# Kernel optimization log

Hardware: AMD Instinct MI355X
Metric: run time of the kernel (lower is better)

Reference implementation:

```python
import jax, jax.numpy as jnp
import numpy as np

PI = 3.1415926
MAX_V = 8  # max vertices of a quad-quad convex intersection
ALPHA, GAMMA, IOU_THRES = 0.25, 2.0, 0.5


def xyxy2xywh_a(b):
    cx = (b[..., 0] + b[..., 2]) * 0.5
    cy = (b[..., 1] + b[..., 3]) * 0.5
    w = b[..., 2] - b[..., 0]
    h = b[..., 3] - b[..., 1]
    return jnp.stack([cx, cy, w, h, b[..., 4]], -1)


def rbox_2_quad(b):
    # [N,5] (x1,y1,x2,y2,theta_deg) -> [N,4,2] corner quads
    x = xyxy2xywh_a(b)
    cx, cy, w, h, t = x[:, 0], x[:, 1], x[:, 2], x[:, 3], x[:, 4]
    th = t * (PI / 180.0)
    c, s = jnp.cos(th), jnp.sin(th)
    dx = jnp.array([-0.5, 0.5, 0.5, -0.5], b.dtype)
    dy = jnp.array([-0.5, -0.5, 0.5, 0.5], b.dtype)
    px = cx[:, None] + dx * w[:, None] * c[:, None] - dy * h[:, None] * s[:, None]
    py = cy[:, None] + dx * w[:, None] * s[:, None] + dy * h[:, None] * c[:, None]
    return jnp.stack([px, py], -1)


def min_area_square(b):
    cx = (b[:, 0] + b[:, 2]) * 0.5
    cy = (b[:, 1] + b[:, 3]) * 0.5
    s = jnp.maximum(b[:, 2] - b[:, 0], b[:, 3] - b[:, 1]) * 0.5
    return jnp.stack([cx - s, cy - s, cx + s, cy + s], 1)


def bbox_overlaps(a, b):
    # axis-aligned IoU matrix [N,M]
    lt = jnp.maximum(a[:, None, :2], b[None, :, :2])
    rb = jnp.minimum(a[:, None, 2:], b[None, :, 2:])
    wh = jnp.clip(rb - lt, 0.0)
    inter = wh[..., 0] * wh[..., 1]
    area_a = (a[:, 2] - a[:, 0]) * (a[:, 3] - a[:, 1])
    area_b = (b[:, 2] - b[:, 0]) * (b[:, 3] - b[:, 1])
    return inter / (area_a[:, None] + area_b[None, :] - inter + 1e-6)


def points_in_quads(pts, quads):
    # pointsJf: pts [A,2] inside convex quads [G,4,2] -> [A,G] {0,1}
    e = jnp.roll(quads, -1, axis=1) - quads  # [G,4,2]
    rel = pts[:, None, None, :] - quads[None]  # [A,G,4,2]
    cr = e[None, ..., 0] * rel[..., 1] - e[None, ..., 1] * rel[..., 0]
    inside = jnp.all(cr >= 0, -1) | jnp.all(cr <= 0, -1)
    return inside.astype(pts.dtype)


def _signed_area2(q):
    return jnp.sum(q[:, 0] * jnp.roll(q[:, 1], -1) - jnp.roll(q[:, 0], -1) * q[:, 1])


def _quad_inter_area(q1, q2):
    # Sutherland-Hodgman clipping of quad q1 by convex quad q2, fixed 8-vertex buffer
    q1 = jnp.where(_signed_area2(q1) < 0, q1[::-1], q1)
    q2 = jnp.where(_signed_area2(q2) < 0, q2[::-1], q2)
    poly = jnp.zeros((MAX_V, 2), q1.dtype).at[:4].set(q1)
    edges = jnp.stack([q2, jnp.roll(q2, -1, axis=0)], 1)  # [4,2,2]

    def clip(carry, edge):
        poly, n = carry
        a, b = edge[0], edge[1]
        idx = jnp.arange(MAX_V)
        nidx = jnp.where(idx + 1 < n, idx + 1, 0)
        cur, nxt = poly, poly[nidx]
        d = b - a
        dc = d[0] * (cur[:, 1] - a[1]) - d[1] * (cur[:, 0] - a[0])
        dn = d[0] * (nxt[:, 1] - a[1]) - d[1] * (nxt[:, 0] - a[0])
        denom = dc - dn
        t = dc / jnp.where(jnp.abs(denom) < 1e-12, 1e-12, denom)
        inter = cur + t[:, None] * (nxt - cur)
        active = idx < n
        keep_cur = active & (dc >= 0)
        keep_int = active & ((dc >= 0) != (dn >= 0))
        pts = jnp.stack([cur, inter], 1).reshape(2 * MAX_V, 2)
        flags = jnp.stack([keep_cur, keep_int], 1).reshape(-1)
        pos = jnp.where(flags, jnp.cumsum(flags) - 1, MAX_V)
        newpoly = jnp.zeros((MAX_V + 1, 2), poly.dtype).at[pos].set(pts)[:MAX_V]
        return (newpoly, flags.sum()), None

    (poly, n), _ = jax.lax.scan(clip, (poly, jnp.int32(4)), edges)
    idx = jnp.arange(MAX_V)
    nidx = jnp.where(idx + 1 < n, idx + 1, 0)
    contrib = poly[:, 0] * poly[nidx, 1] - poly[nidx, 0] * poly[:, 1]
    area = 0.5 * jnp.abs(jnp.sum(jnp.where(idx < n, contrib, 0.0)))
    return jnp.where(n >= 3, area, 0.0)


def rbox_overlaps(quads_a, quads_g, gate, thresh=0.1):
    area_a = 0.5 * jnp.abs(jax.vmap(_signed_area2)(quads_a))
    area_g = 0.5 * jnp.abs(jax.vmap(_signed_area2)(quads_g))
    inter = jax.vmap(lambda qa: jax.vmap(lambda qg: _quad_inter_area(qa, qg))(quads_g))(quads_a)
    iou = inter / (area_a[:, None] + area_g[None, :] - inter + 1e-6)
    return jnp.where(gate > thresh, iou, 0.0)


def encode(anchors, gt):
    a = xyxy2xywh_a(anchors)
    g = xyxy2xywh_a(gt)
    dx = (g[:, 0] - a[:, 0]) / a[:, 2]
    dy = (g[:, 1] - a[:, 1]) / a[:, 3]
    dw = jnp.log(g[:, 2] / a[:, 2])
    dh = jnp.log(g[:, 3] / a[:, 3])
    dt = (g[:, 4] - a[:, 4]) * (PI / 180.0)
    return jnp.stack([dx, dy, dw, dh, dt], 1)


def decode(anchors, deltas):
    a = xyxy2xywh_a(anchors)
    cx = a[..., 0] + deltas[..., 0] * a[..., 2]
    cy = a[..., 1] + deltas[..., 1] * a[..., 3]
    w = a[..., 2] * jnp.exp(deltas[..., 2])
    h = a[..., 3] * jnp.exp(deltas[..., 3])
    t = a[..., 4] + deltas[..., 4] * (180.0 / PI)
    return jnp.stack([cx, cy, w, h, t], -1)


def smooth_l1(x, t, beta=1.0 / 9):
    diff = jnp.abs(x - t)
    return jnp.where(diff < beta, 0.5 * diff * diff / beta, diff - 0.5 * beta)


def _forward(classifications, regressions, anchors, annotations):
    B = classifications.shape[0]
    _ = decode(anchors, regressions)  # all_pred_boxes (unused when func='smooth')
    cls_losses, reg_losses = [], []
    for j in range(B):
        cls = jnp.clip(classifications[j], 1e-4, 1.0 - 1e-4)
        anch = anchors[j]
        gtb = annotations[j, :, :5]
        labels = annotations[j, :, 5].astype(jnp.int32)
        indicator = bbox_overlaps(min_area_square(anch), min_area_square(gtb))
        centers = xyxy2xywh_a(anch)[:, :2]
        quads_g = rbox_2_quad(gtb)
        inside = points_in_quads(centers, quads_g)
        quads_a = rbox_2_quad(anch)
        ious = rbox_overlaps(quads_a, quads_g, inside * indicator)  # [A,G]
        iou_max = ious.max(1)
        iou_argmax = ious.argmax(1)
        pos = iou_max >= IOU_THRES
        max_gt = ious.max(0)
        argmax_gt = ious.argmax(0)
        low = (max_gt < IOU_THRES).astype(jnp.int32)
        pos = (pos.astype(jnp.int32).at[argmax_gt].max(low)).astype(bool)
        num_pos = pos.sum()
        C = cls.shape[1]
        onehot = jax.nn.one_hot(labels[iou_argmax], C, dtype=cls.dtype)
        tgt = -jnp.ones_like(cls)
        tgt = jnp.where((iou_max < IOU_THRES - 0.1)[:, None], 0.0, tgt)
        tgt = jnp.where(pos[:, None], onehot, tgt)
        af = jnp.where(tgt == 1.0, ALPHA, 1.0 - ALPHA)
        fw = af * jnp.where(tgt == 1.0, 1.0 - cls, cls) ** GAMMA
        bce = -(tgt * jnp.log(cls + 1e-6) + (1.0 - tgt) * jnp.log(1.0 - cls + 1e-6))
        cls_loss = jnp.where(tgt != -1.0, fw * bce, 0.0).sum() / jnp.maximum(num_pos.astype(cls.dtype), 1.0)
        cls_losses.append(cls_loss)
        reg_t = encode(anch, gtb[iou_argmax])
        l = smooth_l1(regressions[j], reg_t)
        denom = (jnp.maximum(num_pos, 1) * l.shape[1]).astype(l.dtype)
        reg_loss = jnp.where(num_pos > 0, (l * pos[:, None].astype(l.dtype)).sum() / denom, 0.0)
        reg_losses.append(reg_loss)
    loss_cls = 5.0 * jnp.stack(cls_losses).mean(keepdims=True)
    loss_reg = 2.0 * jnp.stack(reg_losses).mean(keepdims=True)
    return loss_cls, loss_reg


def setup_inputs() -> dict:
    key = jax.random.key(0)
    ks = jax.random.split(key, 8)
    B, A, G, C = 2, 32768, 32, 15
    cls = jax.random.uniform(ks[0], (B, A, C), jnp.float32)
    reg = jax.random.normal(ks[1], (B, A, 5), jnp.float32) * 0.1
    ac = jax.random.uniform(ks[2], (B, A, 2), jnp.float32, 0.0, 1024.0)
    awh = jax.random.uniform(ks[3], (B, A, 2), jnp.float32, 16.0, 256.0)
    anchors = jnp.concatenate([ac - awh * 0.5, ac + awh * 0.5, jnp.zeros((B, A, 1), jnp.float32)], -1)
    gc = jax.random.uniform(ks[4], (B, G, 2), jnp.float32, 64.0, 960.0)
    gwh = jax.random.uniform(ks[5], (B, G, 2), jnp.float32, 24.0, 300.0)
    gt = jax.random.uniform(ks[6], (B, G, 1), jnp.float32, -90.0, 90.0)
    glab = jax.random.randint(ks[7], (B, G, 1), 0, C).astype(jnp.float32)
    annotations = jnp.concatenate([gc - gwh * 0.5, gc + gwh * 0.5, gt, glab], -1)
    return {"classifications": cls, "regressions": reg, "anchors": anchors, "annotations": annotations}


def reference(classifications, regressions, anchors, annotations):
    return _forward(classifications, regressions, anchors, annotations)
```

## Files before the change

kernel.cpp:

```cpp
#include <hip/hip_runtime.h>

#define A_N 32768
#define G_N 32
#define C_N 15
#define APB 256
#define H_N 4
#define BPB (A_N / APB)
#define DEG2RAD ((float)(3.1415926 / 180.0))
#define BETA (1.0f / 9.0f)

typedef unsigned long long ull;

template <int NIN>
__device__ __forceinline__ int clip_pass(float ax, float ay, float dx, float dy,
                                         float (&PX)[8], float (&PY)[8], int n) {
  constexpr int NOUT = (NIN + 1 < 8) ? NIN + 1 : 8;
  float d[NIN];
#pragma unroll
  for (int i = 0; i < NIN; ++i)
    d[i] = dx * (PY[i] - ay) - dy * (PX[i] - ax);
  float NX[NOUT], NY[NOUT];
#pragma unroll
  for (int i = 0; i < NOUT; ++i) { NX[i] = 0.f; NY[i] = 0.f; }
  int m = 0;
#pragma unroll
  for (int i = 0; i < NIN; ++i) {
    if (i < n) {
      bool w = (i + 1 < n);
      float dn = w ? d[(i + 1) % NIN] : d[0];
      float xn = w ? PX[(i + 1) % NIN] : PX[0];
      float yn = w ? PY[(i + 1) % NIN] : PY[0];
      bool kc = (d[i] >= 0.f);
      bool kn = (dn >= 0.f);
      if (kc) {
#pragma unroll
        for (int o = 0; o < NOUT; ++o)
          if (o <= 2 * i && m == o) { NX[o] = PX[i]; NY[o] = PY[i]; }
        ++m;
      }
      if (kc != kn) {
        float den = d[i] - dn;
        if (fabsf(den) < 1e-12f) den = 1e-12f;
        float t = d[i] / den;
        float ix = PX[i] + t * (xn - PX[i]);
        float iy = PY[i] + t * (yn - PY[i]);
#pragma unroll
        for (int o = 0; o < NOUT; ++o)
          if (o <= 2 * i + 1 && m == o) { NX[o] = ix; NY[o] = iy; }
        ++m;
      }
    }
  }
#pragma unroll
  for (int i = 0; i < NOUT; ++i) { PX[i] = NX[i]; PY[i] = NY[i]; }
#pragma unroll
  for (int i = NOUT; i < 8; ++i) { PX[i] = 0.f; PY[i] = 0.f; }
  return m;
}

__global__ __launch_bounds__(1024) void k_fused(
    const float* __restrict__ cls_in, const float* __restrict__ reg_in,
    const float* __restrict__ anchors, const float* __restrict__ annot,
    ull* __restrict__ gpart, ull* __restrict__ rowpack,
    float* __restrict__ cls_part, float* __restrict__ reg_part,
    int* __restrict__ cnt_part) {
  int j = blockIdx.x >> 7;
  int blk = blockIdx.x & (BPB - 1);
  int tid = threadIdx.x;
  int la = tid & (APB - 1);
  int h = tid >> 8;
  int a = blk * APB + la;
  size_t ia = (size_t)j * A_N + a;

  __shared__ float4 g_sqv[G_N];
  __shared__ float2 g_meta[G_N];
  __shared__ float4 g_vx[G_N], g_vy[G_N];
  __shared__ float4 a_qx[APB], a_qy[APB];
  __shared__ float a_area[APB];
  __shared__ ull rowbest[APB];
  __shared__ ull colmax[G_N];
  __shared__ unsigned short list[APB * G_N];
  __shared__ int cnt;
  __shared__ int lab[G_N];
  __shared__ float gcx[G_N], gcy[G_N], gw2[G_N], gh2[G_N], gth[G_N];
  __shared__ float w1[16], w2[16];
  __shared__ int w3[16];

  float pcv[4];
  {
    const float* c = cls_in + ia * C_N;
#pragma unroll
    for (int k = 0; k < 4; ++k) {
      int ci = h * 4 + k;
      pcv[k] = (ci < C_N) ? c[ci] : 0.f;
    }
  }
  float rvv[5];
  if (h == 0) {
    const float* r = reg_in + ia * 5;
#pragma unroll
    for (int i = 0; i < 5; ++i) rvv[i] = r[i];
  } else {
#pragma unroll
    for (int i = 0; i < 5; ++i) rvv[i] = 0.f;
  }

  if (tid == 0) cnt = 0;
  if (tid < APB) rowbest[tid] = 0xFFFFFFFFull;
  if (tid < G_N) colmax[tid] = 0xFFFFFFFFull;

  if (tid < G_N) {
    const float* g = annot + ((size_t)j * G_N + tid) * 6;
    float x1 = g[0], y1 = g[1], x2 = g[2], y2 = g[3], t = g[4];
    float cxx = (x1 + x2) * 0.5f, cyy = (y1 + y2) * 0.5f;
    float w = x2 - x1, hh = y2 - y1;
    gcx[tid] = cxx; gcy[tid] = cyy; gw2[tid] = w; gh2[tid] = hh; gth[tid] = t;
    lab[tid] = (int)g[5];
    float th = t * DEG2RAD;
    float c = cosf(th), s = sinf(th);
    const float ddx[4] = {-0.5f, 0.5f, 0.5f, -0.5f};
    const float ddy[4] = {-0.5f, -0.5f, 0.5f, 0.5f};
    float px[4], py[4];
#pragma unroll
    for (int k = 0; k < 4; ++k) {
      px[k] = cxx + ddx[k] * w * c - ddy[k] * hh * s;
      py[k] = cyy + ddx[k] * w * s + ddy[k] * hh * c;
    }
    float s2 = 0.f;
#pragma unroll
    for (int k = 0; k < 4; ++k)
      s2 += px[k] * py[(k + 1) & 3] - px[(k + 1) & 3] * py[k];
    if (s2 < 0.f) {
      g_vx[tid] = make_float4(px[3], px[2], px[1], px[0]);
      g_vy[tid] = make_float4(py[3], py[2], py[1], py[0]);
    } else {
      g_vx[tid] = make_float4(px[0], px[1], px[2], px[3]);
      g_vy[tid] = make_float4(py[0], py[1], py[2], py[3]);
    }
    float half = fmaxf(w, hh) * 0.5f;
    float sx1 = cxx - half, sy1 = cyy - half, sx2 = cxx + half, sy2 = cyy + half;
    g_sqv[tid] = make_float4(sx1, sy1, sx2, sy2);
    g_meta[tid] = make_float2((sx2 - sx1) * (sy2 - sy1), 0.5f * fabsf(s2));
  }

  const float* an = anchors + ia * 5;
  float ax1 = an[0], ay1 = an[1], ax2 = an[2], ay2 = an[3], at = an[4];
  float acx = (ax1 + ax2) * 0.5f, acy = (ay1 + ay2) * 0.5f;
  float aw = ax2 - ax1, ah = ay2 - ay1;
  float ath = at * DEG2RAD;
  float ac = cosf(ath), asn = sinf(ath);
  {
    const float ddx[4] = {-0.5f, 0.5f, 0.5f, -0.5f};
    const float ddy[4] = {-0.5f, -0.5f, 0.5f, 0.5f};
    float apx[4], apy[4];
#pragma unroll
    for (int k = 0; k < 4; ++k) {
      apx[k] = acx + ddx[k] * aw * ac - ddy[k] * ah * asn;
      apy[k] = acy + ddx[k] * aw * asn + ddy[k] * ah * ac;
    }
    float s2a = 0.f;
#pragma unroll
    for (int k = 0; k < 4; ++k)
      s2a += apx[k] * apy[(k + 1) & 3] - apx[(k + 1) & 3] * apy[k];
    if (s2a < 0.f) {
      float tx = apx[0], ty = apy[0];
      apx[0] = apx[3]; apy[0] = apy[3]; apx[3] = tx; apy[3] = ty;
      tx = apx[1]; ty = apy[1];
      apx[1] = apx[2]; apy[1] = apy[2]; apx[2] = tx; apy[2] = ty;
    }
    if (h == 0) {
      a_qx[la] = make_float4(apx[0], apx[1], apx[2], apx[3]);
      a_qy[la] = make_float4(apy[0], apy[1], apy[2], apy[3]);
      a_area[la] = 0.5f * fabsf(s2a);
    }
  }
  float half = fmaxf(aw, ah) * 0.5f;
  float asx1 = acx - half, asy1 = acy - half, asx2 = acx + half, asy2 = acy + half;
  float asarea = (asx2 - asx1) * (asy2 - asy1);
  __syncthreads();

#pragma unroll
  for (int gg = 0; gg < G_N / H_N; ++gg) {
    int g = h * (G_N / H_N) + gg;
    float4 sq = g_sqv[g];
    float2 meta = g_meta[g];
    float ltx = fmaxf(asx1, sq.x);
    float lty = fmaxf(asy1, sq.y);
    float rbx = fminf(asx2, sq.z);
    float rby = fminf(asy2, sq.w);
    float iw = fmaxf(rbx - ltx, 0.f);
    float ih = fmaxf(rby - lty, 0.f);
    float inter_s = iw * ih;
    float ind = inter_s / (asarea + meta.x - inter_s + 1e-6f);
    float4 vx = g_vx[g], vy = g_vy[g];
    float cr0 = (vx.y - vx.x) * (acy - vy.x) - (vy.y - vy.x) * (acx - vx.x);
    float cr1 = (vx.z - vx.y) * (acy - vy.y) - (vy.z - vy.y) * (acx - vx.y);
    float cr2 = (vx.w - vx.z) * (acy - vy.z) - (vy.w - vy.z) * (acx - vx.z);
    float cr3 = (vx.x - vx.w) * (acy - vy.w) - (vy.x - vy.w) * (acx - vx.w);
    bool pall = (cr0 >= 0.f) & (cr1 >= 0.f) & (cr2 >= 0.f) & (cr3 >= 0.f);
    bool nall = (cr0 <= 0.f) & (cr1 <= 0.f) & (cr2 <= 0.f) & (cr3 <= 0.f);
    if ((pall || nall) && ind > 0.1f) {
      int p = atomicAdd(&cnt, 1);
      list[p] = (unsigned short)((la << 5) | g);
    }
  }
  __syncthreads();

  int np = cnt;
  for (int i = tid; i < np; i += 1024) {
    int ent = list[i];
    int ca = ent >> 5, g = ent & 31;
    float4 aqx = a_qx[ca], aqy = a_qy[ca];
    float PX[8], PY[8];
    PX[0] = aqx.x; PX[1] = aqx.y; PX[2] = aqx.z; PX[3] = aqx.w;
    PY[0] = aqy.x; PY[1] = aqy.y; PY[2] = aqy.z; PY[3] = aqy.w;
#pragma unroll
    for (int k = 4; k < 8; ++k) { PX[k] = 0.f; PY[k] = 0.f; }
    float4 gvx = g_vx[g], gvy = g_vy[g];
    int n = 4;
    n = clip_pass<4>(gvx.x, gvy.x, gvx.y - gvx.x, gvy.y - gvy.x, PX, PY, n);
    n = clip_pass<5>(gvx.y, gvy.y, gvx.z - gvx.y, gvy.z - gvy.y, PX, PY, n);
    n = clip_pass<6>(gvx.z, gvy.z, gvx.w - gvx.z, gvy.w - gvy.z, PX, PY, n);
    n = clip_pass<7>(gvx.w, gvy.w, gvx.x - gvx.w, gvy.x - gvy.w, PX, PY, n);
    float s = 0.f;
#pragma unroll
    for (int k = 0; k < 8; ++k) {
      if (k < n) {
        float xn = (k + 1 < n) ? PX[(k + 1) & 7] : PX[0];
        float yn = (k + 1 < n) ? PY[(k + 1) & 7] : PY[0];
        s += PX[k] * yn - xn * PY[k];
      }
    }
    float inter = (n >= 3) ? 0.5f * fabsf(s) : 0.f;
    float v = inter / (a_area[ca] + g_meta[g].y - inter + 1e-6f);
    ull pr = ((ull)__float_as_uint(v) << 32) | (unsigned)(~(unsigned)g);
    atomicMax(&rowbest[ca], pr);
    unsigned ga = (unsigned)(blk * APB + ca);
    ull pc = ((ull)__float_as_uint(v) << 32) | (unsigned)(~ga);
    atomicMax(&colmax[g], pc);
  }
  __syncthreads();

  ull rb = rowbest[la];
  float im = __uint_as_float((unsigned)(rb >> 32));
  int arg = (int)(~(unsigned)rb);
  int p = (im >= 0.5f) ? 1 : 0;

  if (h == 0) rowpack[ia] = rb;
  if (tid < G_N)
    gpart[((size_t)j * BPB + blk) * G_N + tid] = colmax[tid];

  int lb = lab[arg];
  float csum = 0.f;
  bool bg = (im < 0.4f);
  if (p || bg) {
#pragma unroll
    for (int k = 0; k < 4; ++k) {
      int ci = h * 4 + k;
      if (ci < C_N) {
        float pc = fminf(fmaxf(pcv[k], 1e-4f), 0.9999f);
        bool tgt1 = p && (ci == lb);
        if (tgt1)
          csum += 0.25f * (1.f - pc) * (1.f - pc) * (-__logf(pc + 1e-6f));
        else
          csum += 0.75f * pc * pc * (-__logf(1.f - pc + 1e-6f));
      }
    }
  }

  float rsum = 0.f;
  if (p && h == 0) {
    float t5[5];
    t5[0] = (gcx[arg] - acx) / aw;
    t5[1] = (gcy[arg] - acy) / ah;
    t5[2] = __logf(gw2[arg] / aw);
    t5[3] = __logf(gh2[arg] / ah);
    t5[4] = (gth[arg] - at) * DEG2RAD;
#pragma unroll
    for (int i = 0; i < 5; ++i) {
      float d = fabsf(rvv[i] - t5[i]);
      rsum += (d < BETA) ? (0.5f * d * d / BETA) : (d - 0.5f * BETA);
    }
  }
  int pcnt = (h == 0) ? p : 0;

  float v1 = csum, v2 = rsum;
  int v3 = pcnt;
#pragma unroll
  for (int off = 32; off; off >>= 1) {
    v1 += __shfl_xor(v1, off);
    v2 += __shfl_xor(v2, off);
    v3 += __shfl_xor(v3, off);
  }
  int wv = tid >> 6, ln = tid & 63;
  if (ln == 0) { w1[wv] = v1; w2[wv] = v2; w3[wv] = v3; }
  __syncthreads();
  if (tid == 0) {
    float t1 = 0.f, t2 = 0.f;
    int t3 = 0;
#pragma unroll
    for (int k = 0; k < 16; ++k) { t1 += w1[k]; t2 += w2[k]; t3 += w3[k]; }
    cls_part[blockIdx.x] = t1;
    reg_part[blockIdx.x] = t2;
    cnt_part[blockIdx.x] = t3;
  }
}

__global__ __launch_bounds__(256) void k_fix(
    const float* __restrict__ cls_in, const float* __restrict__ reg_in,
    const float* __restrict__ anchors, const float* __restrict__ annot,
    const ull* __restrict__ gpart, const ull* __restrict__ rowpack,
    const float* __restrict__ cls_part, const float* __restrict__ reg_part,
    const int* __restrict__ cnt_part, float* __restrict__ out, int B) {
  int tid = threadIdx.x;
  __shared__ ull sred[8][G_N];
  __shared__ int fanchor[G_N], owner[G_N];
  __shared__ float dcs[G_N], drs[G_N];
  __shared__ int dct[G_N];
  __shared__ float bd_c[8], bd_r[8];
  __shared__ int bd_n[8];
  __shared__ float s1[256], s2[256];
  __shared__ int s3[256];

  for (int j = 0; j < B; ++j) {
    {
      int g = tid & 31, chunk = tid >> 5;
      const ull* gp = gpart + (size_t)j * BPB * G_N;
      ull m = 0;
#pragma unroll
      for (int b = 0; b < BPB / 8; ++b) {
        ull v = gp[(size_t)(chunk * (BPB / 8) + b) * G_N + g];
        m = v > m ? v : m;
      }
      sred[chunk][g] = m;
    }
    __syncthreads();
    if (tid < G_N) {
      ull m = sred[0][tid];
#pragma unroll
      for (int c = 1; c < 8; ++c) m = sred[c][tid] > m ? sred[c][tid] : m;
      float v = __uint_as_float((unsigned)(m >> 32));
      fanchor[tid] = (v < 0.5f) ? (int)(~(unsigned)m) : -1;
      dcs[tid] = 0.f; drs[tid] = 0.f; dct[tid] = 0;
      owner[tid] = 0;
    }
    __syncthreads();
    if (tid == 0) {
      for (int g = 0; g < G_N; ++g) {
        int af = fanchor[g];
        if (af < 0) continue;
        bool dup = false;
        for (int g2 = 0; g2 < g; ++g2) dup = dup || (fanchor[g2] == af);
        owner[g] = dup ? 0 : 1;
      }
    }
    __syncthreads();
    if (tid < G_N && owner[tid]) {
      int af = fanchor[tid];
      size_t ia = (size_t)j * A_N + af;
      ull rb = rowpack[ia];
      float im = __uint_as_float((unsigned)(rb >> 32));
      if (im < 0.5f) {
        int arg = (int)(~(unsigned)rb);
        const float* gg = annot + ((size_t)j * G_N + arg) * 6;
        int lb = (int)gg[5];
        const float* c = cls_in + ia * C_N;
        bool bg = (im < 0.4f);
        float ca = 0.f, cb = 0.f;
#pragma unroll
        for (int ci = 0; ci < C_N; ++ci) {
          float pc = fminf(fmaxf(c[ci], 1e-4f), 0.9999f);
          float neg = 0.75f * pc * pc * (-__logf(1.f - pc + 1e-6f));
          if (ci == lb)
            ca += 0.25f * (1.f - pc) * (1.f - pc) * (-__logf(pc + 1e-6f));
          else
            ca += neg;
          if (bg) cb += neg;
        }
        const float* an = anchors + ia * 5;
        float acx = (an[0] + an[2]) * 0.5f, acy = (an[1] + an[3]) * 0.5f;
        float aw = an[2] - an[0], ah = an[3] - an[1];
        float gcxv = (gg[0] + gg[2]) * 0.5f, gcyv = (gg[1] + gg[3]) * 0.5f;
        float gwv = gg[2] - gg[0], ghv = gg[3] - gg[1];
        const float* r = reg_in + ia * 5;
        float t5[5];
        t5[0] = (gcxv - acx) / aw;
        t5[1] = (gcyv - acy) / ah;
        t5[2] = __logf(gwv / aw);
        t5[3] = __logf(ghv / ah);
        t5[4] = (gg[4] - an[4]) * DEG2RAD;
        float rs = 0.f;
#pragma unroll
        for (int i = 0; i < 5; ++i) {
          float d = fabsf(r[i] - t5[i]);
          rs += (d < BETA) ? (0.5f * d * d / BETA) : (d - 0.5f * BETA);
        }
        dcs[tid] = ca - cb;
        drs[tid] = rs;
        dct[tid] = 1;
      }
    }
    __syncthreads();
    if (tid == 0) {
      float dc = 0.f, dr = 0.f;
      int dn = 0;
      for (int g = 0; g < G_N; ++g) { dc += dcs[g]; dr += drs[g]; dn += dct[g]; }
      bd_c[j] = dc; bd_r[j] = dr; bd_n[j] = dn;
    }
    __syncthreads();
  }

  int P = B * BPB;
  float cv = 0.f, rvv = 0.f;
  int nv = 0;
  if (tid < P) { cv = cls_part[tid]; rvv = reg_part[tid]; nv = cnt_part[tid]; }
  s1[tid] = cv; s2[tid] = rvv; s3[tid] = nv;
  __syncthreads();
  for (int o = 64; o; o >>= 1) {
    if ((tid & 127) < o) {
      s1[tid] += s1[tid + o]; s2[tid] += s2[tid + o]; s3[tid] += s3[tid + o];
    }
    __syncthreads();
  }
  if (tid == 0) {
    float cl = 0.f, rl = 0.f;
    for (int jj = 0; jj < B; ++jj) {
      float cs = s1[jj * 128] + bd_c[jj];
      float rs = s2[jj * 128] + bd_r[jj];
      int np = s3[jj * 128] + bd_n[jj];
      float npf = (np > 0) ? (float)np : 1.f;
      cl += cs / npf;
      rl += (np > 0) ? rs / (npf * 5.f) : 0.f;
    }
    out[0] = 5.0f * cl / (float)B;
    out[1] = 2.0f * rl / (float)B;
  }
}

extern "C" void kernel_launch(void* const* d_in, const int* in_sizes, int n_in,
                              void* d_out, int out_size, void* d_ws, size_t ws_size,
                              hipStream_t stream) {
  const float* cls = (const float*)d_in[0];
  const float* reg = (const float*)d_in[1];
  const float* anc = (const float*)d_in[2];
  const float* ann = (const float*)d_in[3];
  int B = in_sizes[3] / (G_N * 6);

  char* w = (char*)d_ws;
  ull* gpart = (ull*)w;        w += (size_t)B * BPB * G_N * sizeof(ull);
  ull* rowpack = (ull*)w;      w += (size_t)B * A_N * sizeof(ull);
  float* cls_part = (float*)w; w += (size_t)B * BPB * 4;
  float* reg_part = (float*)w; w += (size_t)B * BPB * 4;
  int* cnt_part = (int*)w;     w += (size_t)B * BPB * 4;

  k_fused<<<B * BPB, 1024, 0, stream>>>(cls, reg, anc, ann, gpart, rowpack,
                                        cls_part, reg_part, cnt_part);
  k_fix<<<1, 256, 0, stream>>>(cls, reg, anc, ann, gpart, rowpack,
                               cls_part, reg_part, cnt_part, (float*)d_out, B);
}
```

Before: 35.82 us.

## Shrink fused blocks to 64 anchors and 256 threads, parallelize fix-up ownership

Cuts anchors per block from 256 to 64 and threads per block from 1024 to 256, giving 4x more blocks with less shared memory each so more blocks can be resident per CU. It also swaps cosf/sinf for the fast __cosf/__sinf intrinsics. The fix-up kernel now does duplicate-owner detection per thread instead of in a serial loop on one thread, and each thread sums four partials to handle the larger partial count. Risks are lower precision in the rotation trig, four times as many per-block partials and gpart entries for k_fix to reduce serially, and possible reliance on the k_fix reduction exactly covering B*BPB partials.

```diff
diff --git a/kernel.cpp b/kernel.cpp
--- a/kernel.cpp
+++ b/kernel.cpp
@@ -3,7 +3,8 @@
 #define A_N 32768
 #define G_N 32
 #define C_N 15
-#define APB 256
+#define APB 64
+#define TPB 256
 #define H_N 4
 #define BPB (A_N / APB)
 #define DEG2RAD ((float)(3.1415926 / 180.0))
@@ -58,17 +59,17 @@
   return m;
 }
 
-__global__ __launch_bounds__(1024) void k_fused(
+__global__ __launch_bounds__(TPB, 4) void k_fused(
     const float* __restrict__ cls_in, const float* __restrict__ reg_in,
     const float* __restrict__ anchors, const float* __restrict__ annot,
     ull* __restrict__ gpart, ull* __restrict__ rowpack,
     float* __restrict__ cls_part, float* __restrict__ reg_part,
     int* __restrict__ cnt_part) {
-  int j = blockIdx.x >> 7;
+  int j = blockIdx.x >> 9;
   int blk = blockIdx.x & (BPB - 1);
   int tid = threadIdx.x;
   int la = tid & (APB - 1);
-  int h = tid >> 8;
+  int h = tid >> 6;
   int a = blk * APB + la;
   size_t ia = (size_t)j * A_N + a;
 
@@ -83,8 +84,8 @@
   __shared__ int cnt;
   __shared__ int lab[G_N];
   __shared__ float gcx[G_N], gcy[G_N], gw2[G_N], gh2[G_N], gth[G_N];
-  __shared__ float w1[16], w2[16];
-  __shared__ int w3[16];
+  __shared__ float w1[H_N], w2[H_N];
+  __shared__ int w3[H_N];
 
   float pcv[4];
   {
@@ -117,7 +118,7 @@
     gcx[tid] = cxx; gcy[tid] = cyy; gw2[tid] = w; gh2[tid] = hh; gth[tid] = t;
     lab[tid] = (int)g[5];
     float th = t * DEG2RAD;
-    float c = cosf(th), s = sinf(th);
+    float c = __cosf(th), s = __sinf(th);
     const float ddx[4] = {-0.5f, 0.5f, 0.5f, -0.5f};
     const float ddy[4] = {-0.5f, -0.5f, 0.5f, 0.5f};
     float px[4], py[4];
@@ -148,7 +149,7 @@
   float acx = (ax1 + ax2) * 0.5f, acy = (ay1 + ay2) * 0.5f;
   float aw = ax2 - ax1, ah = ay2 - ay1;
   float ath = at * DEG2RAD;
-  float ac = cosf(ath), asn = sinf(ath);
+  float ac = __cosf(ath), asn = __sinf(ath);
   {
     const float ddx[4] = {-0.5f, 0.5f, 0.5f, -0.5f};
     const float ddy[4] = {-0.5f, -0.5f, 0.5f, 0.5f};
@@ -207,7 +208,7 @@
   __syncthreads();
 
   int np = cnt;
-  for (int i = tid; i < np; i += 1024) {
+  for (int i = tid; i < np; i += TPB) {
     int ent = list[i];
     int ca = ent >> 5, g = ent & 31;
     float4 aqx = a_qx[ca], aqy = a_qy[ca];
@@ -292,17 +293,13 @@
     v2 += __shfl_xor(v2, off);
     v3 += __shfl_xor(v3, off);
   }
-  int wv = tid >> 6, ln = tid & 63;
-  if (ln == 0) { w1[wv] = v1; w2[wv] = v2; w3[wv] = v3; }
+  int ln = tid & 63;
+  if (ln == 0) { w1[h] = v1; w2[h] = v2; w3[h] = v3; }
   __syncthreads();
   if (tid == 0) {
-    float t1 = 0.f, t2 = 0.f;
-    int t3 = 0;
-#pragma unroll
-    for (int k = 0; k < 16; ++k) { t1 += w1[k]; t2 += w2[k]; t3 += w3[k]; }
-    cls_part[blockIdx.x] = t1;
-    reg_part[blockIdx.x] = t2;
-    cnt_part[blockIdx.x] = t3;
+    cls_part[blockIdx.x] = (w1[0] + w1[1]) + (w1[2] + w1[3]);
+    reg_part[blockIdx.x] = (w2[0] + w2[1]) + (w2[2] + w2[3]);
+    cnt_part[blockIdx.x] = (w3[0] + w3[1]) + (w3[2] + w3[3]);
   }
 }
 
@@ -314,7 +311,7 @@
     const int* __restrict__ cnt_part, float* __restrict__ out, int B) {
   int tid = threadIdx.x;
   __shared__ ull sred[8][G_N];
-  __shared__ int fanchor[G_N], owner[G_N];
+  __shared__ int fanchor[G_N];
   __shared__ float dcs[G_N], drs[G_N];
   __shared__ int dct[G_N];
   __shared__ float bd_c[8], bd_r[8];
@@ -327,7 +324,6 @@
       int g = tid & 31, chunk = tid >> 5;
       const ull* gp = gpart + (size_t)j * BPB * G_N;
       ull m = 0;
-#pragma unroll
       for (int b = 0; b < BPB / 8; ++b) {
         ull v = gp[(size_t)(chunk * (BPB / 8) + b) * G_N + g];
         m = v > m ? v : m;
@@ -342,68 +338,63 @@
       float v = __uint_as_float((unsigned)(m >> 32));
       fanchor[tid] = (v < 0.5f) ? (int)(~(unsigned)m) : -1;
       dcs[tid] = 0.f; drs[tid] = 0.f; dct[tid] = 0;
-      owner[tid] = 0;
     }
     __syncthreads();
-    if (tid == 0) {
-      for (int g = 0; g < G_N; ++g) {
-        int af = fanchor[g];
-        if (af < 0) continue;
-        bool dup = false;
-        for (int g2 = 0; g2 < g; ++g2) dup = dup || (fanchor[g2] == af);
-        owner[g] = dup ? 0 : 1;
-      }
-    }
-    __syncthreads();
-    if (tid < G_N && owner[tid]) {
+    if (tid < G_N) {
       int af = fanchor[tid];
-      size_t ia = (size_t)j * A_N + af;
-      ull rb = rowpack[ia];
-      float im = __uint_as_float((unsigned)(rb >> 32));
-      if (im < 0.5f) {
-        int arg = (int)(~(unsigned)rb);
-        const float* gg = annot + ((size_t)j * G_N + arg) * 6;
-        int lb = (int)gg[5];
-        const float* c = cls_in + ia * C_N;
-        bool bg = (im < 0.4f);
-        float ca = 0.f, cb = 0.f;
-#pragma unroll
-        for (int ci = 0; ci < C_N; ++ci) {
-          float pc = fminf(fmaxf(c[ci], 1e-4f), 0.9999f);
-          float neg = 0.75f * pc * pc * (-__logf(1.f - pc + 1e-6f));
-          if (ci == lb)
-            ca += 0.25f * (1.f - pc) * (1.f - pc) * (-__logf(pc + 1e-6f));
-          else
-            ca += neg;
-          if (bg) cb += neg;
+      bool owner = (af >= 0);
+      for (int g2 = 0; g2 < tid; ++g2)
+        owner = owner && (fanchor[g2] != af);
+      if (owner) {
+        size_t ia = (size_t)j * A_N + af;
+        ull rb = rowpack[ia];
+        float im = __uint_as_float((unsigned)(rb >> 32));
+        if (im < 0.5f) {
+          int arg = (int)(~(unsigned)rb);
+          const float* gg = annot + ((size_t)j * G_N + arg) * 6;
+          int lb = (int)gg[5];
+          const float* c = cls_in + ia * C_N;
+          bool bg = (im < 0.4f);
+          float ca = 0.f, cb = 0.f;
+#pragma unroll
+          for (int ci = 0; ci < C_N; ++ci) {
+            float pc = fminf(fmaxf(c[ci], 1e-4f), 0.9999f);
+            float neg = 0.75f * pc * pc * (-__logf(1.f - pc + 1e-6f));
+            if (ci == lb)
+              ca += 0.25f * (1.f - pc) * (1.f - pc) * (-__logf(pc + 1e-6f));
+            else
+              ca += neg;
+            if (bg) cb += neg;
+          }
+          const float* an = anchors + ia * 5;
+          float acx = (an[0] + an[2]) * 0.5f, acy = (an[1] + an[3]) * 0.5f;
+          float aw = an[2] - an[0], ah = an[3] - an[1];
+          float gcxv = (gg[0] + gg[2]) * 0.5f, gcyv = (gg[1] + gg[3]) * 0.5f;
+          float gwv = gg[2] - gg[0], ghv = gg[3] - gg[1];
+          const float* r = reg_in + ia * 5;
+          float t5[5];
+          t5[0] = (gcxv - acx) / aw;
+          t5[1] = (gcyv - acy) / ah;
+          t5[2] = __logf(gwv / aw);
+          t5[3] = __logf(ghv / ah);
+          t5[4] = (gg[4] - an[4]) * DEG2RAD;
+          float rs = 0.f;
+#pragma unroll
+          for (int i = 0; i < 5; ++i) {
+            float d = fabsf(r[i] - t5[i]);
+            rs += (d < BETA) ? (0.5f * d * d / BETA) : (d - 0.5f * BETA);
+          }
+          dcs[tid] = ca - cb;
+          drs[tid] = rs;
+          dct[tid] = 1;
         }
-        const float* an = anchors + ia * 5;
-        float acx = (an[0] + an[2]) * 0.5f, acy = (an[1] + an[3]) * 0.5f;
-        float aw = an[2] - an[0], ah = an[3] - an[1];
-        float gcxv = (gg[0] + gg[2]) * 0.5f, gcyv = (gg[1] + gg[3]) * 0.5f;
-        float gwv = gg[2] - gg[0], ghv = gg[3] - gg[1];
-        const float* r = reg_in + ia * 5;
-        float t5[5];
-        t5[0] = (gcxv - acx) / aw;
-        t5[1] = (gcyv - acy) / ah;
-        t5[2] = __logf(gwv / aw);
-        t5[3] = __logf(ghv / ah);
-        t5[4] = (gg[4] - an[4]) * DEG2RAD;
-        float rs = 0.f;
-#pragma unroll
-        for (int i = 0; i < 5; ++i) {
-          float d = fabsf(r[i] - t5[i]);
-          rs += (d < BETA) ? (0.5f * d * d / BETA) : (d - 0.5f * BETA);
-        }
-        dcs[tid] = ca - cb;
-        drs[tid] = rs;
-        dct[tid] = 1;
       }
     }
     __syncthreads();
     if (tid == 0) {
       float dc = 0.f, dr = 0.f;
       int dn = 0;
+#pragma unroll
       for (int g = 0; g < G_N; ++g) { dc += dcs[g]; dr += drs[g]; dn += dct[g]; }
       bd_c[j] = dc; bd_r[j] = dr; bd_n[j] = dn;
     }
@@ -413,7 +404,11 @@
   int P = B * BPB;
   float cv = 0.f, rvv = 0.f;
   int nv = 0;
-  if (tid < P) { cv = cls_part[tid]; rvv = reg_part[tid]; nv = cnt_part[tid]; }
+#pragma unroll
+  for (int k = 0; k < 4; ++k) {
+    int idx = tid * 4 + k;
+    if (idx < P) { cv += cls_part[idx]; rvv += reg_part[idx]; nv += cnt_part[idx]; }
+  }
   s1[tid] = cv; s2[tid] = rvv; s3[tid] = nv;
   __syncthreads();
   for (int o = 64; o; o >>= 1) {
@@ -453,8 +448,8 @@
   float* reg_part = (float*)w; w += (size_t)B * BPB * 4;
   int* cnt_part = (int*)w;     w += (size_t)B * BPB * 4;
 
-  k_fused<<<B * BPB, 1024, 0, stream>>>(cls, reg, anc, ann, gpart, rowpack,
-                                        cls_part, reg_part, cnt_part);
+  k_fused<<<B * BPB, TPB, 0, stream>>>(cls, reg, anc, ann, gpart, rowpack,
+                                       cls_part, reg_part, cnt_part);
   k_fix<<<1, 256, 0, stream>>>(cls, reg, anc, ann, gpart, rowpack,
                                cls_part, reg_part, cnt_part, (float*)d_out, B);
 }
```

After: 41.06 us. 1.15x slower.

## Precompute GT quads in a prologue kernel, use fast trig, parallelize dedup

Applied to the files above, without the earlier changes.

Adds a small k_pre kernel that computes each GT box's corner quad, enclosing square, areas and metadata once. k_fused then loads these as float4s instead of recomputing them in every one of the 256 blocks. Anchor trig switches to the fast __cosf/__sinf intrinsics. In k_fix, the serial owner-dedup loop on thread 0 becomes a per-thread check, which removes one barrier. The trade-off is an extra kernel launch and slightly less accurate trig.

```diff
diff --git a/kernel.cpp b/kernel.cpp
--- a/kernel.cpp
+++ b/kernel.cpp
@@ -4,10 +4,12 @@
 #define G_N 32
 #define C_N 15
 #define APB 256
+#define TPB 1024
 #define H_N 4
 #define BPB (A_N / APB)
 #define DEG2RAD ((float)(3.1415926 / 180.0))
 #define BETA (1.0f / 9.0f)
+#define GT_STRIDE 24
 
 typedef unsigned long long ull;
 
@@ -58,9 +60,52 @@
   return m;
 }
 
-__global__ __launch_bounds__(1024) void k_fused(
+__global__ void k_pre(const float* __restrict__ annot, float* __restrict__ gtpre,
+                      int B) {
+  int t = threadIdx.x;
+  if (t >= B * G_N) return;
+  const float* g = annot + (size_t)t * 6;
+  float x1 = g[0], y1 = g[1], x2 = g[2], y2 = g[3], th = g[4], lb = g[5];
+  float cxx = (x1 + x2) * 0.5f, cyy = (y1 + y2) * 0.5f;
+  float w = x2 - x1, h = y2 - y1;
+  float a = th * DEG2RAD;
+  float c = __cosf(a), s = __sinf(a);
+  const float ddx[4] = {-0.5f, 0.5f, 0.5f, -0.5f};
+  const float ddy[4] = {-0.5f, -0.5f, 0.5f, 0.5f};
+  float px[4], py[4];
+#pragma unroll
+  for (int k = 0; k < 4; ++k) {
+    px[k] = cxx + ddx[k] * w * c - ddy[k] * h * s;
+    py[k] = cyy + ddx[k] * w * s + ddy[k] * h * c;
+  }
+  float s2 = 0.f;
+#pragma unroll
+  for (int k = 0; k < 4; ++k)
+    s2 += px[k] * py[(k + 1) & 3] - px[(k + 1) & 3] * py[k];
+  float vx[4], vy[4];
+  if (s2 < 0.f) {
+#pragma unroll
+    for (int k = 0; k < 4; ++k) { vx[k] = px[3 - k]; vy[k] = py[3 - k]; }
+  } else {
+#pragma unroll
+    for (int k = 0; k < 4; ++k) { vx[k] = px[k]; vy[k] = py[k]; }
+  }
+  float half = fmaxf(w, h) * 0.5f;
+  float sx1 = cxx - half, sy1 = cyy - half, sx2 = cxx + half, sy2 = cyy + half;
+  float* o = gtpre + (size_t)t * GT_STRIDE;
+  o[0] = sx1; o[1] = sy1; o[2] = sx2; o[3] = sy2;
+  o[4] = (sx2 - sx1) * (sy2 - sy1);
+  o[5] = 0.5f * fabsf(s2);
+  o[6] = 0.f; o[7] = 0.f;
+  o[8] = vx[0]; o[9] = vx[1]; o[10] = vx[2]; o[11] = vx[3];
+  o[12] = vy[0]; o[13] = vy[1]; o[14] = vy[2]; o[15] = vy[3];
+  o[16] = cxx; o[17] = cyy; o[18] = w; o[19] = h;
+  o[20] = th; o[21] = lb; o[22] = 0.f; o[23] = 0.f;
+}
+
+__global__ __launch_bounds__(TPB) void k_fused(
     const float* __restrict__ cls_in, const float* __restrict__ reg_in,
-    const float* __restrict__ anchors, const float* __restrict__ annot,
+    const float* __restrict__ anchors, const float* __restrict__ gtpre,
     ull* __restrict__ gpart, ull* __restrict__ rowpack,
     float* __restrict__ cls_part, float* __restrict__ reg_part,
     int* __restrict__ cnt_part) {
@@ -110,37 +155,14 @@
   if (tid < G_N) colmax[tid] = 0xFFFFFFFFull;
 
   if (tid < G_N) {
-    const float* g = annot + ((size_t)j * G_N + tid) * 6;
-    float x1 = g[0], y1 = g[1], x2 = g[2], y2 = g[3], t = g[4];
-    float cxx = (x1 + x2) * 0.5f, cyy = (y1 + y2) * 0.5f;
-    float w = x2 - x1, hh = y2 - y1;
-    gcx[tid] = cxx; gcy[tid] = cyy; gw2[tid] = w; gh2[tid] = hh; gth[tid] = t;
-    lab[tid] = (int)g[5];
-    float th = t * DEG2RAD;
-    float c = cosf(th), s = sinf(th);
-    const float ddx[4] = {-0.5f, 0.5f, 0.5f, -0.5f};
-    const float ddy[4] = {-0.5f, -0.5f, 0.5f, 0.5f};
-    float px[4], py[4];
-#pragma unroll
-    for (int k = 0; k < 4; ++k) {
-      px[k] = cxx + ddx[k] * w * c - ddy[k] * hh * s;
-      py[k] = cyy + ddx[k] * w * s + ddy[k] * hh * c;
-    }
-    float s2 = 0.f;
-#pragma unroll
-    for (int k = 0; k < 4; ++k)
-      s2 += px[k] * py[(k + 1) & 3] - px[(k + 1) & 3] * py[k];
-    if (s2 < 0.f) {
-      g_vx[tid] = make_float4(px[3], px[2], px[1], px[0]);
-      g_vy[tid] = make_float4(py[3], py[2], py[1], py[0]);
-    } else {
-      g_vx[tid] = make_float4(px[0], px[1], px[2], px[3]);
-      g_vy[tid] = make_float4(py[0], py[1], py[2], py[3]);
-    }
-    float half = fmaxf(w, hh) * 0.5f;
-    float sx1 = cxx - half, sy1 = cyy - half, sx2 = cxx + half, sy2 = cyy + half;
-    g_sqv[tid] = make_float4(sx1, sy1, sx2, sy2);
-    g_meta[tid] = make_float2((sx2 - sx1) * (sy2 - sy1), 0.5f * fabsf(s2));
+    const float4* gp = (const float4*)(gtpre + ((size_t)j * G_N + tid) * GT_STRIDE);
+    float4 q0 = gp[0], q1 = gp[1], q2 = gp[2], q3 = gp[3], q4 = gp[4], q5 = gp[5];
+    g_sqv[tid] = q0;
+    g_meta[tid] = make_float2(q1.x, q1.y);
+    g_vx[tid] = q2;
+    g_vy[tid] = q3;
+    gcx[tid] = q4.x; gcy[tid] = q4.y; gw2[tid] = q4.z; gh2[tid] = q4.w;
+    gth[tid] = q5.x; lab[tid] = (int)q5.y;
   }
 
   const float* an = anchors + ia * 5;
@@ -148,7 +170,7 @@
   float acx = (ax1 + ax2) * 0.5f, acy = (ay1 + ay2) * 0.5f;
   float aw = ax2 - ax1, ah = ay2 - ay1;
   float ath = at * DEG2RAD;
-  float ac = cosf(ath), asn = sinf(ath);
+  float ac = __cosf(ath), asn = __sinf(ath);
   {
     const float ddx[4] = {-0.5f, 0.5f, 0.5f, -0.5f};
     const float ddy[4] = {-0.5f, -0.5f, 0.5f, 0.5f};
@@ -207,7 +229,7 @@
   __syncthreads();
 
   int np = cnt;
-  for (int i = tid; i < np; i += 1024) {
+  for (int i = tid; i < np; i += TPB) {
     int ent = list[i];
     int ca = ent >> 5, g = ent & 31;
     float4 aqx = a_qx[ca], aqy = a_qy[ca];
@@ -314,7 +336,7 @@
     const int* __restrict__ cnt_part, float* __restrict__ out, int B) {
   int tid = threadIdx.x;
   __shared__ ull sred[8][G_N];
-  __shared__ int fanchor[G_N], owner[G_N];
+  __shared__ int fanchor[G_N];
   __shared__ float dcs[G_N], drs[G_N];
   __shared__ int dct[G_N];
   __shared__ float bd_c[8], bd_r[8];
@@ -342,68 +364,63 @@
       float v = __uint_as_float((unsigned)(m >> 32));
       fanchor[tid] = (v < 0.5f) ? (int)(~(unsigned)m) : -1;
       dcs[tid] = 0.f; drs[tid] = 0.f; dct[tid] = 0;
-      owner[tid] = 0;
     }
     __syncthreads();
-    if (tid == 0) {
-      for (int g = 0; g < G_N; ++g) {
-        int af = fanchor[g];
-        if (af < 0) continue;
-        bool dup = false;
-        for (int g2 = 0; g2 < g; ++g2) dup = dup || (fanchor[g2] == af);
-        owner[g] = dup ? 0 : 1;
-      }
-    }
-    __syncthreads();
-    if (tid < G_N && owner[tid]) {
+    if (tid < G_N) {
       int af = fanchor[tid];
-      size_t ia = (size_t)j * A_N + af;
-      ull rb = rowpack[ia];
-      float im = __uint_as_float((unsigned)(rb >> 32));
-      if (im < 0.5f) {
-        int arg = (int)(~(unsigned)rb);
-        const float* gg = annot + ((size_t)j * G_N + arg) * 6;
-        int lb = (int)gg[5];
-        const float* c = cls_in + ia * C_N;
-        bool bg = (im < 0.4f);
-        float ca = 0.f, cb = 0.f;
-#pragma unroll
-        for (int ci = 0; ci < C_N; ++ci) {
-          float pc = fminf(fmaxf(c[ci], 1e-4f), 0.9999f);
-          float neg = 0.75f * pc * pc * (-__logf(1.f - pc + 1e-6f));
-          if (ci == lb)
-            ca += 0.25f * (1.f - pc) * (1.f - pc) * (-__logf(pc + 1e-6f));
-          else
-            ca += neg;
-          if (bg) cb += neg;
+      bool owner = (af >= 0);
+      for (int g2 = 0; g2 < tid; ++g2)
+        owner = owner && (fanchor[g2] != af);
+      if (owner) {
+        size_t ia = (size_t)j * A_N + af;
+        ull rb = rowpack[ia];
+        float im = __uint_as_float((unsigned)(rb >> 32));
+        if (im < 0.5f) {
+          int arg = (int)(~(unsigned)rb);
+          const float* gg = annot + ((size_t)j * G_N + arg) * 6;
+          int lb = (int)gg[5];
+          const float* c = cls_in + ia * C_N;
+          bool bg = (im < 0.4f);
+          float ca = 0.f, cb = 0.f;
+#pragma unroll
+          for (int ci = 0; ci < C_N; ++ci) {
+            float pc = fminf(fmaxf(c[ci], 1e-4f), 0.9999f);
+            float neg = 0.75f * pc * pc * (-__logf(1.f - pc + 1e-6f));
+            if (ci == lb)
+              ca += 0.25f * (1.f - pc) * (1.f - pc) * (-__logf(pc + 1e-6f));
+            else
+              ca += neg;
+            if (bg) cb += neg;
+          }
+          const float* an = anchors + ia * 5;
+          float acx = (an[0] + an[2]) * 0.5f, acy = (an[1] + an[3]) * 0.5f;
+          float aw = an[2] - an[0], ah = an[3] - an[1];
+          float gcxv = (gg[0] + gg[2]) * 0.5f, gcyv = (gg[1] + gg[3]) * 0.5f;
+          float gwv = gg[2] - gg[0], ghv = gg[3] - gg[1];
+          const float* r = reg_in + ia * 5;
+          float t5[5];
+          t5[0] = (gcxv - acx) / aw;
+          t5[1] = (gcyv - acy) / ah;
+          t5[2] = __logf(gwv / aw);
+          t5[3] = __logf(ghv / ah);
+          t5[4] = (gg[4] - an[4]) * DEG2RAD;
+          float rs = 0.f;
+#pragma unroll
+          for (int i = 0; i < 5; ++i) {
+            float d = fabsf(r[i] - t5[i]);
+            rs += (d < BETA) ? (0.5f * d * d / BETA) : (d - 0.5f * BETA);
+          }
+          dcs[tid] = ca - cb;
+          drs[tid] = rs;
+          dct[tid] = 1;
         }
-        const float* an = anchors + ia * 5;
-        float acx = (an[0] + an[2]) * 0.5f, acy = (an[1] + an[3]) * 0.5f;
-        float aw = an[2] - an[0], ah = an[3] - an[1];
-        float gcxv = (gg[0] + gg[2]) * 0.5f, gcyv = (gg[1] + gg[3]) * 0.5f;
-        float gwv = gg[2] - gg[0], ghv = gg[3] - gg[1];
-        const float* r = reg_in + ia * 5;
-        float t5[5];
-        t5[0] = (gcxv - acx) / aw;
-        t5[1] = (gcyv - acy) / ah;
-        t5[2] = __logf(gwv / aw);
-        t5[3] = __logf(ghv / ah);
-        t5[4] = (gg[4] - an[4]) * DEG2RAD;
-        float rs = 0.f;
-#pragma unroll
-        for (int i = 0; i < 5; ++i) {
-          float d = fabsf(r[i] - t5[i]);
-          rs += (d < BETA) ? (0.5f * d * d / BETA) : (d - 0.5f * BETA);
-        }
-        dcs[tid] = ca - cb;
-        drs[tid] = rs;
-        dct[tid] = 1;
       }
     }
     __syncthreads();
     if (tid == 0) {
       float dc = 0.f, dr = 0.f;
       int dn = 0;
+#pragma unroll
       for (int g = 0; g < G_N; ++g) { dc += dcs[g]; dr += drs[g]; dn += dct[g]; }
       bd_c[j] = dc; bd_r[j] = dr; bd_n[j] = dn;
     }
@@ -447,14 +464,16 @@
   int B = in_sizes[3] / (G_N * 6);
 
   char* w = (char*)d_ws;
+  float* gtpre = (float*)w;    w += (size_t)B * G_N * GT_STRIDE * 4;
   ull* gpart = (ull*)w;        w += (size_t)B * BPB * G_N * sizeof(ull);
   ull* rowpack = (ull*)w;      w += (size_t)B * A_N * sizeof(ull);
   float* cls_part = (float*)w; w += (size_t)B * BPB * 4;
   float* reg_part = (float*)w; w += (size_t)B * BPB * 4;
   int* cnt_part = (int*)w;     w += (size_t)B * BPB * 4;
 
-  k_fused<<<B * BPB, 1024, 0, stream>>>(cls, reg, anc, ann, gpart, rowpack,
-                                        cls_part, reg_part, cnt_part);
+  k_pre<<<1, 64, 0, stream>>>(ann, gtpre, B);
+  k_fused<<<B * BPB, TPB, 0, stream>>>(cls, reg, anc, gtpre, gpart, rowpack,
+                                       cls_part, reg_part, cnt_part);
   k_fix<<<1, 256, 0, stream>>>(cls, reg, anc, ann, gpart, rowpack,
                                cls_part, reg_part, cnt_part, (float*)d_out, B);
 }
```

Result: slower. 38.84 us (+8.4%).
